# Optimization experiments

Measured on AMD Instinct MI355X. Metric: run time of the kernel, lower is better.

Reference implementation:

```python
import jax, jax.numpy as jnp
import numpy as np

N = 50000
E = 800000
L = 0.7
EPS = 1e-12  # torch F.normalize eps


def setup_inputs() -> dict:
    key = jax.random.key(0)
    k1, k2, k3, k4, k5 = jax.random.split(key, 5)
    x = jax.random.normal(k1, (N, 256), dtype=jnp.float32)
    W = jax.random.normal(k2, (256, 128), dtype=jnp.float32) * 0.05
    b = jax.random.normal(k3, (128,), dtype=jnp.float32) * 0.05
    src = jax.random.randint(k4, (E,), 0, N, dtype=jnp.int32)
    dst = jax.random.randint(k5, (E,), 0, N, dtype=jnp.int32)
    return {"x": x, "W": W, "b": b, "src": src, "dst": dst}


def _mean_agg(h, src, dst, denom):
    # DGL copy_u + mean over in-edges: mean_{e:(u->v)} h[u]; zero for isolated nodes
    s = jax.ops.segment_sum(h[src], dst, num_segments=N)  # [N, D]
    return s / denom


def reference(x, W, b, src, dst):
    # MLP: Linear -> relu -> row-wise L2 normalize
    h = jax.nn.relu(x @ W + b)
    h = h / jnp.maximum(jnp.linalg.norm(h, axis=1, keepdims=True), EPS)
    # in-degree for mean (clamped to 1 so isolated nodes give 0, matching DGL)
    deg = jax.ops.segment_sum(jnp.ones((E,), jnp.float32), dst, num_segments=N)
    denom = jnp.maximum(deg, 1.0)[:, None]  # [N,1]
    neigh1 = _mean_agg(h, src, dst, denom)
    neigh2 = _mean_agg(neigh1, src, dst, denom)
    mean_h = L * neigh1 + (1.0 - L) * neigh2
    return (h, mean_h)
```

## Files before the change

kernel.cpp:

```cpp
#include <hip/hip_runtime.h>

#define D_IN 256
#define D_OUT 128
#define NBINS 256
#define NB 256

typedef short bf16x8 __attribute__((ext_vector_type(8)));
typedef float f32x4 __attribute__((ext_vector_type(4)));

__device__ __forceinline__ unsigned short f2bf(float f) {
    unsigned int u = __float_as_uint(f);
    unsigned int r = (u + 0x7FFFu + ((u >> 16) & 1u)) >> 16;
    return (unsigned short)r;
}
__device__ __forceinline__ unsigned int pack2(float a, float b) {
    return (unsigned int)f2bf(a) | ((unsigned int)f2bf(b) << 16);
}
__device__ __forceinline__ void gload_lds16(const void* g, void* l) {
    __builtin_amdgcn_global_load_lds(
        (const __attribute__((address_space(1))) void*)g,
        (__attribute__((address_space(3))) void*)l, 16, 0, 0);
}

__global__ __launch_bounds__(256) void k_wt_b1(const float* __restrict__ W,
                                               unsigned short* __restrict__ wt,
                                               const int* __restrict__ dst, int E, int epb,
                                               int* __restrict__ blockbase) {
    __shared__ int hist[NBINS];
    int t = threadIdx.x;
    if (t < 128) {
        int idx = blockIdx.x * 128 + t;
        wt[idx] = f2bf(W[(idx & 255) * D_OUT + (idx >> 8)]);
    }
    hist[t] = 0;
    __syncthreads();
    int s = blockIdx.x * epb;
    int e = min(s + epb, E);
    for (int i = s + t; i < e; i += 256)
        atomicAdd(&hist[dst[i] >> 8], 1);
    __syncthreads();
    blockbase[blockIdx.x * NBINS + t] = hist[t];
}

__global__ __launch_bounds__(256) void k_csrmlp(
    const int* __restrict__ src, const int* __restrict__ dst, int E, int epb,
    const int* __restrict__ blockbase, int* __restrict__ coarse_cnt,
    int* __restrict__ coarse_base, int* __restrict__ ebuf,
    const float* __restrict__ x, const unsigned short* __restrict__ wt,
    const float* __restrict__ bias, float* __restrict__ h,
    unsigned char* __restrict__ hq, int n, int nmblk) {
    __shared__ char smem[32768];
    const int tid = threadIdx.x;
    const int bid = blockIdx.x;

    if (bid < NB) {
        int* cur  = (int*)smem;
        int* base = (int*)(smem + 1024);
        int* sd   = (int*)(smem + 2048);
        int run = 0, myprefix = 0;
        #pragma unroll 8
        for (int b = 0; b < NB; ++b) {
            int v = blockbase[b * NBINS + tid];
            if (b == bid) myprefix = run;
            run += v;
        }
        sd[tid] = run;
        cur[tid] = 0;
        __syncthreads();
        for (int off = 1; off < 256; off <<= 1) {
            int v = (tid >= off) ? sd[tid - off] : 0;
            __syncthreads();
            sd[tid] += v;
            __syncthreads();
        }
        int cb_excl = sd[tid] - run;
        base[tid] = cb_excl + myprefix;
        if (bid == 0) { coarse_cnt[tid] = run; coarse_base[tid] = cb_excl; }
        __syncthreads();
        const int s = bid * epb, e = min(s + epb, E);
        for (int i = s + tid; i < e; i += 256) {
            int d = dst[i];
            int bin = d >> 8;
            int p = atomicAdd(&cur[bin], 1);
            ebuf[base[bin] + p] = (src[i] & 0xffff) | ((d & 255) << 16);
        }
        return;
    }

    const int tile = bid - NB;
    if (tile >= nmblk) return;
    float* sx = (float*)smem;
    unsigned short* swc = (unsigned short*)(smem + 16384);
    const int wid  = tid >> 6;
    const int lane = tid & 63;
    const int row0 = tile * 64;

    f32x4 acc[8];
    #pragma unroll
    for (int fn = 0; fn < 8; ++fn) acc[fn] = (f32x4){0.f, 0.f, 0.f, 0.f};

    for (int k0 = 0; k0 < D_IN; k0 += 64) {
        __syncthreads();
        #pragma unroll
        for (int i = 0; i < 4; ++i) {
            int bi = i * 4 + wid;
            int chunk = bi * 64 + lane;
            int r  = chunk >> 4;
            int cs = chunk & 15;
            int grow = row0 + r;
            const float* g = x + (size_t)grow * D_IN + k0 + ((cs ^ (r & 7)) << 2);
            if (grow < n) gload_lds16(g, (char*)sx + bi * 1024);
        }
        #pragma unroll
        for (int i = 0; i < 4; ++i) {
            int bi = i * 4 + wid;
            int chunk = bi * 64 + lane;
            int nr = chunk >> 3;
            int cs = chunk & 7;
            const unsigned short* g = wt + nr * D_IN + k0 + ((cs ^ (nr & 7)) << 3);
            gload_lds16(g, (char*)swc + bi * 1024);
        }
        __syncthreads();

        #pragma unroll
        for (int kk = 0; kk < 2; ++kk) {
            int r  = wid * 16 + (lane & 15);
            int cs = kk * 8 + (lane >> 4) * 2;
            float4 a0 = *reinterpret_cast<const float4*>(sx + r * 64 + ((cs ^ (r & 7)) << 2));
            float4 a1 = *reinterpret_cast<const float4*>(sx + r * 64 + (((cs + 1) ^ (r & 7)) << 2));
            union { unsigned int u[4]; bf16x8 v; } af;
            af.u[0] = pack2(a0.x, a0.y);
            af.u[1] = pack2(a0.z, a0.w);
            af.u[2] = pack2(a1.x, a1.y);
            af.u[3] = pack2(a1.z, a1.w);
            #pragma unroll
            for (int fn = 0; fn < 8; ++fn) {
                int nr = fn * 16 + (lane & 15);
                int cb = kk * 4 + (lane >> 4);
                bf16x8 bfrag = *reinterpret_cast<const bf16x8*>(
                    swc + nr * 64 + ((cb ^ (nr & 7)) << 3));
                acc[fn] = __builtin_amdgcn_mfma_f32_16x16x32_bf16(af.v, bfrag, acc[fn], 0, 0, 0);
            }
        }
    }

    float bias_r[8];
    #pragma unroll
    for (int fn = 0; fn < 8; ++fn) bias_r[fn] = bias[fn * 16 + (lane & 15)];
    const int colbase = lane & 15;
    const int rgrp = lane >> 4;
    #pragma unroll
    for (int reg = 0; reg < 4; ++reg) {
        int grow = row0 + wid * 16 + rgrp * 4 + reg;
        float v[8];
        float ss = 0.f;
        #pragma unroll
        for (int fn = 0; fn < 8; ++fn) {
            float t = fmaxf(acc[fn][reg] + bias_r[fn], 0.f);
            v[fn] = t;
            ss += t * t;
        }
        ss += __shfl_xor(ss, 1);
        ss += __shfl_xor(ss, 2);
        ss += __shfl_xor(ss, 4);
        ss += __shfl_xor(ss, 8);
        float sc = 1.f / fmaxf(sqrtf(ss), 1e-12f);
        if (grow < n) {
            #pragma unroll
            for (int fn = 0; fn < 8; ++fn) {
                float o = v[fn] * sc;
                h[(size_t)grow * D_OUT + fn * 16 + colbase] = o;
                hq[(size_t)grow * D_OUT + fn * 16 + colbase] =
                    (unsigned char)(int)rintf(o * 255.f);
            }
        }
    }
}

__global__ __launch_bounds__(512) void k_b4(const int* __restrict__ ebuf,
                                            const int* __restrict__ coarse_cnt,
                                            const int* __restrict__ coarse_base,
                                            int* __restrict__ deg, int* __restrict__ offs,
                                            int* __restrict__ csr, int n) {
    __shared__ int hist[NBINS];
    __shared__ int lo[NBINS];
    const int t = threadIdx.x;
    const int bin = blockIdx.x;
    const int base = coarse_base[bin];
    const int size = coarse_cnt[bin];
    if (t < 256) hist[t] = 0;
    __syncthreads();
    for (int i = t; i < size; i += 512)
        atomicAdd(&hist[(ebuf[base + i] >> 16) & 255], 1);
    __syncthreads();
    int hh = 0;
    if (t < 256) { hh = hist[t]; lo[t] = hh; }
    __syncthreads();
    for (int off = 1; off < 256; off <<= 1) {
        int v = (t >= off && t < 256) ? lo[t - off] : 0;
        __syncthreads();
        if (t < 256) lo[t] += v;
        __syncthreads();
    }
    if (t < 256) {
        int excl = lo[t] - hh;
        int gdst = bin * 256 + t;
        if (gdst < n) { deg[gdst] = hh; offs[gdst] = base + excl; }
        hist[t] = excl;
    }
    __syncthreads();
    for (int i = t; i < size; i += 512) {
        int pr = ebuf[base + i];
        int p = atomicAdd(&hist[(pr >> 16) & 255], 1);
        csr[base + p] = pr & 0xffff;
    }
}

__global__ __launch_bounds__(256) void k_agg1(const unsigned char* __restrict__ hq,
                                              const int* __restrict__ offs,
                                              const int* __restrict__ deg,
                                              const int* __restrict__ csr,
                                              unsigned char* __restrict__ n1q, int n) {
    int node = (blockIdx.x * blockDim.x + threadIdx.x) >> 4;
    int sub  = threadIdx.x & 15;
    if (node >= n) return;
    int d = deg[node];
    int s = offs[node], e = s + d;
    unsigned int a0 = 0u, a1 = 0u, a2 = 0u, a3 = 0u;
    int i = s;
    for (; i + 7 < e; i += 8) {
        #pragma unroll
        for (int j = 0; j < 8; ++j) {
            int u = csr[i + j];
            uint2 q = *reinterpret_cast<const uint2*>(hq + (size_t)u * D_OUT + sub * 8);
            a0 += q.x & 0x00FF00FFu;
            a1 += (q.x >> 8) & 0x00FF00FFu;
            a2 += q.y & 0x00FF00FFu;
            a3 += (q.y >> 8) & 0x00FF00FFu;
        }
    }
    for (; i < e; ++i) {
        int u = csr[i];
        uint2 q = *reinterpret_cast<const uint2*>(hq + (size_t)u * D_OUT + sub * 8);
        a0 += q.x & 0x00FF00FFu;
        a1 += (q.x >> 8) & 0x00FF00FFu;
        a2 += q.y & 0x00FF00FFu;
        a3 += (q.y >> 8) & 0x00FF00FFu;
    }
    float inv = 1.f / (float)max(d, 1);
    unsigned int b0 = (unsigned int)(int)rintf((float)(a0 & 0xffffu) * inv);
    unsigned int b1 = (unsigned int)(int)rintf((float)(a1 & 0xffffu) * inv);
    unsigned int b2 = (unsigned int)(int)rintf((float)(a0 >> 16) * inv);
    unsigned int b3 = (unsigned int)(int)rintf((float)(a1 >> 16) * inv);
    unsigned int b4 = (unsigned int)(int)rintf((float)(a2 & 0xffffu) * inv);
    unsigned int b5 = (unsigned int)(int)rintf((float)(a3 & 0xffffu) * inv);
    unsigned int b6 = (unsigned int)(int)rintf((float)(a2 >> 16) * inv);
    unsigned int b7 = (unsigned int)(int)rintf((float)(a3 >> 16) * inv);
    uint2 o;
    o.x = b0 | (b1 << 8) | (b2 << 16) | (b3 << 24);
    o.y = b4 | (b5 << 8) | (b6 << 16) | (b7 << 24);
    *reinterpret_cast<uint2*>(n1q + (size_t)node * D_OUT + sub * 8) = o;
}

__global__ __launch_bounds__(256) void k_agg2(const unsigned char* __restrict__ n1q,
                                              const int* __restrict__ offs,
                                              const int* __restrict__ deg,
                                              const int* __restrict__ csr,
                                              float* __restrict__ out_m, int n) {
    int node = (blockIdx.x * blockDim.x + threadIdx.x) >> 4;
    int sub  = threadIdx.x & 15;
    if (node >= n) return;
    int d = deg[node];
    int s = offs[node], e = s + d;
    unsigned int a0 = 0u, a1 = 0u, a2 = 0u, a3 = 0u;
    int i = s;
    for (; i + 7 < e; i += 8) {
        #pragma unroll
        for (int j = 0; j < 8; ++j) {
            int u = csr[i + j];
            uint2 q = *reinterpret_cast<const uint2*>(n1q + (size_t)u * D_OUT + sub * 8);
            a0 += q.x & 0x00FF00FFu;
            a1 += (q.x >> 8) & 0x00FF00FFu;
            a2 += q.y & 0x00FF00FFu;
            a3 += (q.y >> 8) & 0x00FF00FFu;
        }
    }
    for (; i < e; ++i) {
        int u = csr[i];
        uint2 q = *reinterpret_cast<const uint2*>(n1q + (size_t)u * D_OUT + sub * 8);
        a0 += q.x & 0x00FF00FFu;
        a1 += (q.x >> 8) & 0x00FF00FFu;
        a2 += q.y & 0x00FF00FFu;
        a3 += (q.y >> 8) & 0x00FF00FFu;
    }
    float inv = 1.f / (float)max(d, 1);
    uint2 own = *reinterpret_cast<const uint2*>(n1q + (size_t)node * D_OUT + sub * 8);
    const float s255 = 1.f / 255.f;
    float4 o0, o1;
    o0.x = (0.7f * (float)(own.x & 0xffu)         + 0.3f * (float)(a0 & 0xffffu) * inv) * s255;
    o0.y = (0.7f * (float)((own.x >> 8) & 0xffu)  + 0.3f * (float)(a1 & 0xffffu) * inv) * s255;
    o0.z = (0.7f * (float)((own.x >> 16) & 0xffu) + 0.3f * (float)(a0 >> 16) * inv) * s255;
    o0.w = (0.7f * (float)(own.x >> 24)           + 0.3f * (float)(a1 >> 16) * inv) * s255;
    o1.x = (0.7f * (float)(own.y & 0xffu)         + 0.3f * (float)(a2 & 0xffffu) * inv) * s255;
    o1.y = (0.7f * (float)((own.y >> 8) & 0xffu)  + 0.3f * (float)(a3 & 0xffffu) * inv) * s255;
    o1.z = (0.7f * (float)((own.y >> 16) & 0xffu) + 0.3f * (float)(a2 >> 16) * inv) * s255;
    o1.w = (0.7f * (float)(own.y >> 24)           + 0.3f * (float)(a3 >> 16) * inv) * s255;
    float* op = out_m + (size_t)node * D_OUT + sub * 8;
    *reinterpret_cast<float4*>(op)     = o0;
    *reinterpret_cast<float4*>(op + 4) = o1;
}

static inline size_t align_up(size_t v, size_t a) { return (v + a - 1) & ~(a - 1); }

extern "C" void kernel_launch(void* const* d_in, const int* in_sizes, int n_in,
                              void* d_out, int out_size, void* d_ws, size_t ws_size,
                              hipStream_t stream) {
    const float* x  = (const float*)d_in[0];
    const float* W  = (const float*)d_in[1];
    const float* b  = (const float*)d_in[2];
    const int* src  = (const int*)d_in[3];
    const int* dst  = (const int*)d_in[4];

    const int n = in_sizes[0] / D_IN;
    const int E = in_sizes[3];

    float* out_h = (float*)d_out;
    float* out_m = out_h + (size_t)n * D_OUT;

    char* ws = (char*)d_ws;
    size_t off = 0;
    int* coarse_cnt  = (int*)(ws + off); off = align_up(off + NBINS * 4, 256);
    int* coarse_base = (int*)(ws + off); off = align_up(off + NBINS * 4, 256);
    int* blockbase   = (int*)(ws + off); off = align_up(off + (size_t)NBINS * NB * 4, 256);
    int* ebuf        = (int*)(ws + off); off = align_up(off + (size_t)E * 4, 256);
    int* csr         = (int*)(ws + off); off = align_up(off + (size_t)E * 4, 256);
    int* deg         = (int*)(ws + off); off = align_up(off + (size_t)n * 4, 256);
    int* offs        = (int*)(ws + off); off = align_up(off + (size_t)n * 4, 256);
    unsigned short* wt = (unsigned short*)(ws + off); off = align_up(off + (size_t)D_OUT * D_IN * 2, 256);
    unsigned char* hq  = (unsigned char*)(ws + off); off = align_up(off + (size_t)n * D_OUT, 256);
    unsigned char* n1q = (unsigned char*)(ws + off); off = align_up(off + (size_t)n * D_OUT, 256);
    (void)ws_size;

    const int epb = (E + NB - 1) / NB;
    const int nbuckets = (n + 255) / 256;
    const int nmblk = (n + 63) / 64;

    k_wt_b1<<<NB, 256, 0, stream>>>(W, wt, dst, E, epb, blockbase);
    k_csrmlp<<<NB + nmblk, 256, 0, stream>>>(src, dst, E, epb, blockbase,
                                             coarse_cnt, coarse_base, ebuf,
                                             x, wt, b, out_h, hq, n, nmblk);
    k_b4<<<nbuckets, 512, 0, stream>>>(ebuf, coarse_cnt, coarse_base, deg, offs, csr, n);

    const int agg_blocks = (n + 15) / 16;
    k_agg1<<<agg_blocks, 256, 0, stream>>>(hq, offs, deg, csr, n1q, n);
    k_agg2<<<agg_blocks, 256, 0, stream>>>(n1q, offs, deg, csr, out_m, n);
}
```

Measured before the change: 92.66 us.

## Double-buffer MLP GEMM LDS stages with async loads over K

Splits the GEMM K loop into eight 32-wide stages with ping-pong LDS buffers, issuing the next stage's global-to-LDS loads before computing the current one and using explicit vmcnt waits and barriers instead of full syncthreads. The aim is to hide global load latency behind MFMA work in the dense projection part of the fused kernel. Out-of-range rows are now clamped to the last row instead of skipped, and the weight transpose kernel is changed to read W coalesced and scatter the writes. The cost is more barriers per tile and reliance on hand-counted vmcnt values being correct.

```diff
diff --git a/kernel.cpp b/kernel.cpp
--- a/kernel.cpp
+++ b/kernel.cpp
@@ -29,8 +29,10 @@
     __shared__ int hist[NBINS];
     int t = threadIdx.x;
     if (t < 128) {
-        int idx = blockIdx.x * 128 + t;
-        wt[idx] = f2bf(W[(idx & 255) * D_OUT + (idx >> 8)]);
+        int lin = blockIdx.x * 128 + t;
+        int k  = lin >> 7;
+        int nn = lin & 127;
+        wt[nn * 256 + k] = f2bf(W[lin]);
     }
     hist[t] = 0;
     __syncthreads();
@@ -89,8 +91,6 @@
 
     const int tile = bid - NB;
     if (tile >= nmblk) return;
-    float* sx = (float*)smem;
-    unsigned short* swc = (unsigned short*)(smem + 16384);
     const int wid  = tid >> 6;
     const int lane = tid & 63;
     const int row0 = tile * 64;
@@ -99,50 +99,66 @@
     #pragma unroll
     for (int fn = 0; fn < 8; ++fn) acc[fn] = (f32x4){0.f, 0.f, 0.f, 0.f};
 
-    for (int k0 = 0; k0 < D_IN; k0 += 64) {
-        __syncthreads();
+    #define STAGE(p)                                                                   \
+    {                                                                                  \
+        const int k0s = (p) * 32;                                                      \
+        char* sxb = smem + ((p) & 1) * 8192;                                           \
+        char* swb = smem + 16384 + ((p) & 1) * 8192;                                   \
+        _Pragma("unroll")                                                              \
+        for (int i = 0; i < 2; ++i) {                                                  \
+            int bi = i * 4 + wid;                                                      \
+            int chunk = bi * 64 + lane;                                                \
+            int r  = chunk >> 3;                                                       \
+            int cs = chunk & 7;                                                        \
+            int grow = min(row0 + r, n - 1);                                           \
+            const float* g = x + (size_t)grow * D_IN + k0s + ((cs ^ (r & 7)) << 2);    \
+            gload_lds16(g, sxb + bi * 1024);                                           \
+        }                                                                              \
+        _Pragma("unroll")                                                              \
+        for (int i = 0; i < 2; ++i) {                                                  \
+            int bi = i * 4 + wid;                                                      \
+            int chunk = bi * 64 + lane;                                                \
+            int nr = chunk >> 2;                                                       \
+            int cs = chunk & 3;                                                        \
+            const unsigned short* g = wt + nr * D_IN + k0s + ((cs ^ (nr & 3)) << 3);   \
+            gload_lds16(g, swb + bi * 1024);                                           \
+        }                                                                              \
+    }
+
+    STAGE(0);
+    #pragma unroll
+    for (int p = 0; p < 8; ++p) {
+        if (p < 7) {
+            STAGE(p + 1);
+            asm volatile("s_waitcnt vmcnt(4)" ::: "memory");
+        } else {
+            asm volatile("s_waitcnt vmcnt(0)" ::: "memory");
+        }
+        __builtin_amdgcn_s_barrier();
+
+        const float* sxb = (const float*)(smem + (p & 1) * 8192);
+        const unsigned short* swb =
+            (const unsigned short*)(smem + 16384 + (p & 1) * 8192);
+        int r  = wid * 16 + (lane & 15);
+        int cs = (lane >> 4) * 2;
+        float4 a0 = *reinterpret_cast<const float4*>(sxb + r * 32 + ((cs ^ (r & 7)) << 2));
+        float4 a1 = *reinterpret_cast<const float4*>(sxb + r * 32 + (((cs + 1) ^ (r & 7)) << 2));
+        union { unsigned int u[4]; bf16x8 v; } af;
+        af.u[0] = pack2(a0.x, a0.y);
+        af.u[1] = pack2(a0.z, a0.w);
+        af.u[2] = pack2(a1.x, a1.y);
+        af.u[3] = pack2(a1.z, a1.w);
         #pragma unroll
-        for (int i = 0; i < 4; ++i) {
-            int bi = i * 4 + wid;
-            int chunk = bi * 64 + lane;
-            int r  = chunk >> 4;
-            int cs = chunk & 15;
-            int grow = row0 + r;
-            const float* g = x + (size_t)grow * D_IN + k0 + ((cs ^ (r & 7)) << 2);
-            if (grow < n) gload_lds16(g, (char*)sx + bi * 1024);
-        }
-        #pragma unroll
-        for (int i = 0; i < 4; ++i) {
-            int bi = i * 4 + wid;
-            int chunk = bi * 64 + lane;
-            int nr = chunk >> 3;
-            int cs = chunk & 7;
-            const unsigned short* g = wt + nr * D_IN + k0 + ((cs ^ (nr & 7)) << 3);
-            gload_lds16(g, (char*)swc + bi * 1024);
-        }
-        __syncthreads();
-
-        #pragma unroll
-        for (int kk = 0; kk < 2; ++kk) {
-            int r  = wid * 16 + (lane & 15);
-            int cs = kk * 8 + (lane >> 4) * 2;
-            float4 a0 = *reinterpret_cast<const float4*>(sx + r * 64 + ((cs ^ (r & 7)) << 2));
-            float4 a1 = *reinterpret_cast<const float4*>(sx + r * 64 + (((cs + 1) ^ (r & 7)) << 2));
-            union { unsigned int u[4]; bf16x8 v; } af;
-            af.u[0] = pack2(a0.x, a0.y);
-            af.u[1] = pack2(a0.z, a0.w);
-            af.u[2] = pack2(a1.x, a1.y);
-            af.u[3] = pack2(a1.z, a1.w);
-            #pragma unroll
-            for (int fn = 0; fn < 8; ++fn) {
-                int nr = fn * 16 + (lane & 15);
-                int cb = kk * 4 + (lane >> 4);
-                bf16x8 bfrag = *reinterpret_cast<const bf16x8*>(
-                    swc + nr * 64 + ((cb ^ (nr & 7)) << 3));
-                acc[fn] = __builtin_amdgcn_mfma_f32_16x16x32_bf16(af.v, bfrag, acc[fn], 0, 0, 0);
-            }
-        }
-    }
+        for (int fn = 0; fn < 8; ++fn) {
+            int nr = fn * 16 + (lane & 15);
+            int cb = lane >> 4;
+            bf16x8 bfrag = *reinterpret_cast<const bf16x8*>(
+                swb + nr * 32 + ((cb ^ (nr & 3)) << 3));
+            acc[fn] = __builtin_amdgcn_mfma_f32_16x16x32_bf16(af.v, bfrag, acc[fn], 0, 0, 0);
+        }
+        if (p < 7) __builtin_amdgcn_s_barrier();
+    }
+    #undef STAGE
 
     float bias_r[8];
     #pragma unroll
```

New measurement: 92.23 us. About the same (-0.5%).
